# Optimization experiments

Measured on AMD Instinct MI355X. Metric: run time of the kernel, lower is better.

The kernel has to match this reference:

```python
import jax, jax.numpy as jnp
import numpy as np
from jax import lax

B, L, D_MODEL, N_LAYERS = 2, 1024, 768, 2
D_STATE, D_CONV, EXPAND = 16, 4, 2
ED = EXPAND * D_MODEL          # d_inner = 1536
DT_RANK = D_MODEL // 16        # 48
VOCAB = 32000                  # already multiple of 8


def setup_inputs() -> dict:
    key = jax.random.key(0)
    ks = jax.random.split(key, 12)
    s = 0.02
    # dt bias init: inverse-softplus of dt ~ LogUniform(dt_min, dt_max)
    dt = jnp.exp(jax.random.uniform(ks[0], (N_LAYERS, ED)) * (np.log(0.1) - np.log(0.001)) + np.log(0.001))
    dt = jnp.clip(dt, 1e-4)
    dt_b = dt + jnp.log(-jnp.expm1(-dt))
    A_log = jnp.tile(jnp.log(jnp.arange(1, D_STATE + 1, dtype=jnp.float32))[None, None, :], (N_LAYERS, ED, 1))
    return {
        "input_ids": jax.random.randint(ks[1], (B, L), 0, VOCAB),
        "embedding": jax.random.normal(ks[2], (VOCAB, D_MODEL)) * s,
        "ln_w": jnp.ones((N_LAYERS, D_MODEL)),
        "in_proj": jax.random.normal(ks[3], (N_LAYERS, 2 * ED, D_MODEL)) * s,
        "conv_w": jax.random.normal(ks[4], (N_LAYERS, ED, D_CONV)) * (1.0 / np.sqrt(D_CONV)),
        "conv_b": jnp.zeros((N_LAYERS, ED)),
        "x_proj": jax.random.normal(ks[5], (N_LAYERS, DT_RANK + 2 * D_STATE, ED)) * s,
        "dt_w": jax.random.normal(ks[6], (N_LAYERS, ED, DT_RANK)) * (DT_RANK ** -0.5),
        "dt_b": dt_b,
        "A_log": A_log,
        "skip_D": jnp.ones((N_LAYERS, ED)),
        "out_proj": jax.random.normal(ks[7], (N_LAYERS, D_MODEL, ED)) * s,
        "normf_w": jnp.ones((D_MODEL,)),
        "lm_head": jax.random.normal(ks[8], (VOCAB, D_MODEL)) * s,
    }


def _rmsnorm(x, w, eps=1e-5):
    return x * lax.rsqrt(jnp.mean(x * x, axis=-1, keepdims=True) + eps) * w


def _silu(x):
    return x * jax.nn.sigmoid(x)


def _mamba_layer(x, ln, w_in, cw, cb, w_x, wdt, bdt, a_log, d_skip, w_out):
    # x: (B, L, D)
    h = _rmsnorm(x, ln)
    xz = h @ w_in.T                               # (B, L, 2*ED)
    xi, z = xz[..., :ED], xz[..., ED:]
    # depthwise causal conv over time
    xc = jnp.pad(xi.transpose(0, 2, 1), ((0, 0), (0, 0), (D_CONV - 1, 0)))  # (B, ED, L+pad)
    xc = lax.conv_general_dilated(xc, cw[:, None, :], (1,), 'VALID',
                                  feature_group_count=ED,
                                  dimension_numbers=('NCH', 'OIH', 'NCH'))
    xi = _silu((xc + cb[None, :, None]).transpose(0, 2, 1))  # (B, L, ED)
    # input-dependent SSM params
    dbc = xi @ w_x.T                              # (B, L, dt_rank + 2N)
    delta_r = dbc[..., :DT_RANK]
    Bm = dbc[..., DT_RANK:DT_RANK + D_STATE]      # (B, L, N)
    Cm = dbc[..., DT_RANK + D_STATE:]             # (B, L, N)
    delta = jax.nn.softplus(delta_r @ wdt.T + bdt)  # (B, L, ED)
    A = -jnp.exp(a_log)                           # (ED, N)
    dA = jnp.exp(delta[..., None] * A)            # (B, L, ED, N)
    dBx = (delta * xi)[..., None] * Bm[:, :, None, :]  # (B, L, ED, N)

    def step(hc, t):
        dA_t, dBx_t, C_t = t
        hc = dA_t * hc + dBx_t                    # (B, ED, N)
        y = jnp.einsum('ben,bn->be', hc, C_t)
        return hc, y

    h0 = jnp.zeros((x.shape[0], ED, D_STATE), x.dtype)
    _, ys = lax.scan(step, h0, (dA.transpose(1, 0, 2, 3), dBx.transpose(1, 0, 2, 3), Cm.transpose(1, 0, 2)))
    y = ys.transpose(1, 0, 2) + d_skip * xi       # (B, L, ED)
    y = y * _silu(z)
    return x + y @ w_out.T                        # residual


def reference(input_ids, embedding, ln_w, in_proj, conv_w, conv_b, x_proj, dt_w, dt_b, A_log, skip_D, out_proj, normf_w, lm_head):
    x = embedding[input_ids]                      # (B, L, D)
    for i in range(N_LAYERS):
        x = _mamba_layer(x, ln_w[i], in_proj[i], conv_w[i], conv_b[i], x_proj[i],
                         dt_w[i], dt_b[i], A_log[i], skip_D[i], out_proj[i])
    x = _rmsnorm(x, normf_w)
    return x @ lm_head.T                          # (B, L, VOCAB)
```

## Files before the change

### kernel.cpp

```cpp
#include <hip/hip_runtime.h>
#include <hip/hip_bf16.h>

#define BB 2
#define LL 1024
#define DM 768
#define ED 1536
#define NTOK 2048
#define DSTATE 16
#define DTRANK 48
#define VOCAB 32000

#define CHUNK 64
#define NCHUNK (LL / CHUNK)

typedef unsigned short ushort_t;
typedef __attribute__((ext_vector_type(8))) short short8;
typedef __attribute__((ext_vector_type(4))) float f32x4;

__device__ __forceinline__ ushort_t f2bf(float f) {
    __hip_bfloat16 h = __float2bfloat16(f);
    return *(ushort_t*)&h;
}
__device__ __forceinline__ float silu(float x) { return x / (1.f + expf(-x)); }

__global__ void embed_kernel(const int* __restrict__ ids, const float* __restrict__ emb,
                             float* __restrict__ x) {
    int t = blockIdx.x;
    const float* src = emb + (size_t)ids[t] * DM;
    float* dst = x + (size_t)t * DM;
    for (int c = threadIdx.x; c < DM; c += blockDim.x) dst[c] = src[c];
}

__global__ void rmsnorm_kernel(const float* __restrict__ x, const float* __restrict__ w,
                               ushort_t* __restrict__ out, int D) {
    int t = blockIdx.x;
    const float* xr = x + (size_t)t * D;
    float ss = 0.f;
    for (int c = threadIdx.x; c < D; c += blockDim.x) { float v = xr[c]; ss += v * v; }
    #pragma unroll
    for (int o = 32; o > 0; o >>= 1) ss += __shfl_down(ss, o, 64);
    __shared__ float s[4];
    int wid = threadIdx.x >> 6;
    if ((threadIdx.x & 63) == 0) s[wid] = ss;
    __syncthreads();
    float rs = rsqrtf((s[0] + s[1] + s[2] + s[3]) / (float)D + 1e-5f);
    ushort_t* orow = out + (size_t)t * D;
    for (int c = threadIdx.x; c < D; c += blockDim.x)
        orow[c] = f2bf(xr[c] * rs * w[c]);
}

__global__ void w2bf_kernel(const float* __restrict__ w, ushort_t* __restrict__ o) {
    size_t i = ((size_t)blockIdx.x * blockDim.x + threadIdx.x) * 4;
    float4 f = *(const float4*)&w[i];
    ushort4 u;
    u.x = f2bf(f.x); u.y = f2bf(f.y); u.z = f2bf(f.z); u.w = f2bf(f.w);
    *(ushort4*)&o[i] = u;
}

template<bool RESID>
__global__ __launch_bounds__(256) void gemm_bt2(const ushort_t* __restrict__ A,
                                                const ushort_t* __restrict__ Wb,
                                                const float* X, float* out,
                                                int N, int K) {
    __shared__ __align__(16) ushort_t As[128 * 32];
    __shared__ __align__(16) ushort_t Bs[128 * 32];
    const int q = gridDim.x >> 3;
    const int f = (blockIdx.x & 7) * q + (blockIdx.x >> 3);
    const int m0 = (f & 15) * 128;
    const int n0 = (f >> 4) * 128;
    const int tid = threadIdx.x;
    const int w = tid >> 6, lane = tid & 63;
    const int wm = (w >> 1) * 64, wn = (w & 1) * 64;
    const int lrow = lane & 15, koff = (lane >> 4) * 8;
    const int srow = tid >> 2, scol = (tid & 3) * 8;
    const ushort_t* Ab = A  + (size_t)(m0 + srow) * K + scol;
    const ushort_t* Bb = Wb + (size_t)(n0 + srow) * K + scol;

    f32x4 acc[4][4] = {};

    for (int k0 = 0; k0 < K; k0 += 32) {
        uint4 a0 = *(const uint4*)(Ab + k0);
        uint4 a1 = *(const uint4*)(Ab + (size_t)64 * K + k0);
        uint4 b0 = *(const uint4*)(Bb + k0);
        uint4 b1 = *(const uint4*)(Bb + (size_t)64 * K + k0);
        __syncthreads();
        *(uint4*)&As[tid * 8]        = a0;
        *(uint4*)&As[2048 + tid * 8] = a1;
        *(uint4*)&Bs[tid * 8]        = b0;
        *(uint4*)&Bs[2048 + tid * 8] = b1;
        __syncthreads();
        short8 af[4], bfr[4];
        #pragma unroll
        for (int t = 0; t < 4; ++t) af[t]  = *(const short8*)&As[(wm + t * 16 + lrow) * 32 + koff];
        #pragma unroll
        for (int t = 0; t < 4; ++t) bfr[t] = *(const short8*)&Bs[(wn + t * 16 + lrow) * 32 + koff];
        #pragma unroll
        for (int tm = 0; tm < 4; ++tm)
            #pragma unroll
            for (int tn = 0; tn < 4; ++tn)
                acc[tm][tn] = __builtin_amdgcn_mfma_f32_16x16x32_bf16(af[tm], bfr[tn], acc[tm][tn], 0, 0, 0);
    }

    const int kq4 = (lane >> 4) * 4;
    #pragma unroll
    for (int tm = 0; tm < 4; ++tm) {
        #pragma unroll
        for (int tn = 0; tn < 4; ++tn) {
            const int c  = n0 + wn + tn * 16 + lrow;
            const int rb = m0 + wm + tm * 16 + kq4;
            #pragma unroll
            for (int i = 0; i < 4; ++i) {
                size_t off = (size_t)(rb + i) * N + c;
                float v = acc[tm][tn][i];
                if (RESID) v += X[off];
                out[off] = v;
            }
        }
    }
}

__global__ void conv_silu_kernel(const float* __restrict__ xz, const float* __restrict__ cw,
                                 const float* __restrict__ cb, float* __restrict__ xi) {
    int idx = blockIdx.x * blockDim.x + threadIdx.x;
    int c = idx % ED;
    int t = idx / ED;
    int l = t % LL;
    float acc = cb[c];
    #pragma unroll
    for (int k = 0; k < 4; ++k) {
        int ls = l + k - 3;
        if (ls >= 0) acc += xz[(size_t)(t + k - 3) * (2 * ED) + c] * cw[c * 4 + k];
    }
    xi[idx] = silu(acc);
}

__global__ void xproj_kernel(const float* __restrict__ xi, const float* __restrict__ wx,
                             float* __restrict__ dbc) {
    int t = blockIdx.x;
    __shared__ float sx[ED];
    const float* xr = xi + (size_t)t * ED;
    for (int c = threadIdx.x; c < ED; c += blockDim.x) sx[c] = xr[c];
    __syncthreads();
    int w = threadIdx.x >> 6, lane = threadIdx.x & 63;
    for (int j = w; j < DTRANK + 2 * DSTATE; j += 4) {
        const float* wr = wx + (size_t)j * ED;
        float s = 0.f;
        for (int k = lane; k < ED; k += 64) s += sx[k] * wr[k];
        #pragma unroll
        for (int o = 32; o > 0; o >>= 1) s += __shfl_down(s, o, 64);
        if (lane == 0) dbc[(size_t)t * 80 + j] = s;
    }
}

__global__ void dtproj_kernel(const float* __restrict__ dbc, const float* __restrict__ wdt,
                              const float* __restrict__ bdt, float* __restrict__ delta) {
    int t = blockIdx.x;
    __shared__ float sdr[DTRANK];
    if (threadIdx.x < DTRANK) sdr[threadIdx.x] = dbc[(size_t)t * 80 + threadIdx.x];
    __syncthreads();
    for (int e = threadIdx.x; e < ED; e += blockDim.x) {
        const float* wr = wdt + (size_t)e * DTRANK;
        float acc = bdt[e];
        #pragma unroll
        for (int r = 0; r < DTRANK; ++r) acc += sdr[r] * wr[r];
        delta[(size_t)t * ED + e] = (acc > 20.f) ? acc : log1pf(expf(acc));
    }
}


__global__ void scan_chunk_kernel(const float* __restrict__ delta, const float* __restrict__ xi,
                                  const float* __restrict__ dbc, const float* __restrict__ a_log,
                                  const float* __restrict__ skd, float* __restrict__ y,
                                  float* __restrict__ hfin, float* __restrict__ cA) {
    int b = blockIdx.z, c = blockIdx.y;
    int w = threadIdx.x >> 6, lane = threadIdx.x & 63;
    int n = lane & 15;
    int e = blockIdx.x * 16 + w * 4 + (lane >> 4);
    float Ae = -expf(a_log[e * DSTATE + n]);
    float skip = skd[e];
    float h = 0.f, sumdl = 0.f;
    size_t tb = (size_t)b * LL + (size_t)c * CHUNK;
    for (int l = 0; l < CHUNK; ++l) {
        size_t row = tb + l;
        float dl = delta[row * ED + e];
        float xv = xi[row * ED + e];
        float Bv = dbc[row * 80 + DTRANK + n];
        float Cv = dbc[row * 80 + DTRANK + DSTATE + n];
        float dA = __expf(dl * Ae);
        h = dA * h + dl * xv * Bv;
        sumdl += dl;
        float p = h * Cv;
        p += __shfl_xor(p, 1, 16);
        p += __shfl_xor(p, 2, 16);
        p += __shfl_xor(p, 4, 16);
        p += __shfl_xor(p, 8, 16);
        if (n == 0) y[row * ED + e] = p + skip * xv;
    }
    size_t sidx = (((size_t)b * NCHUNK + c) * ED + e) * DSTATE + n;
    hfin[sidx] = h;
    cA[sidx] = __expf(Ae * sumdl);
}

__global__ void chunk_carry_kernel(const float* __restrict__ hfin, const float* __restrict__ cA,
                                   float* __restrict__ hin) {
    int gid = blockIdx.x * blockDim.x + threadIdx.x;
    int b = gid / (ED * DSTATE);
    int rem = gid - b * (ED * DSTATE);
    float h = 0.f;
    for (int c = 0; c < NCHUNK; ++c) {
        size_t idx = ((size_t)(b * NCHUNK + c)) * (ED * DSTATE) + rem;
        hin[idx] = h;
        h = cA[idx] * h + hfin[idx];
    }
}

__global__ void scan_fixup_kernel(const float* __restrict__ delta, const float* __restrict__ dbc,
                                  const float* __restrict__ a_log, const float* __restrict__ hin,
                                  float* __restrict__ y) {
    int b = blockIdx.z, c = blockIdx.y + 1;
    int w = threadIdx.x >> 6, lane = threadIdx.x & 63;
    int n = lane & 15;
    int e = blockIdx.x * 16 + w * 4 + (lane >> 4);
    float Ae = -expf(a_log[e * DSTATE + n]);
    float h0 = hin[(((size_t)b * NCHUNK + c) * ED + e) * DSTATE + n];
    float sumdl = 0.f;
    size_t tb = (size_t)b * LL + (size_t)c * CHUNK;
    for (int l = 0; l < CHUNK; ++l) {
        size_t row = tb + l;
        float dl = delta[row * ED + e];
        sumdl += dl;
        float Cv = dbc[row * 80 + DTRANK + DSTATE + n];
        float p = __expf(Ae * sumdl) * h0 * Cv;
        p += __shfl_xor(p, 1, 16);
        p += __shfl_xor(p, 2, 16);
        p += __shfl_xor(p, 4, 16);
        p += __shfl_xor(p, 8, 16);
        if (n == 0) y[row * ED + e] += p;
    }
}

__global__ void gate_kernel(const float* __restrict__ y, const float* __restrict__ xz,
                            ushort_t* __restrict__ yzb) {
    int idx = blockIdx.x * blockDim.x + threadIdx.x;
    int c = idx % ED;
    int t = idx / ED;
    float z = xz[(size_t)t * (2 * ED) + ED + c];
    yzb[idx] = f2bf(y[idx] * silu(z));
}

extern "C" void kernel_launch(void* const* d_in, const int* in_sizes, int n_in,
                              void* d_out, int out_size, void* d_ws, size_t ws_size,
                              hipStream_t stream) {
    const int*   ids      = (const int*)d_in[0];
    const float* emb      = (const float*)d_in[1];
    const float* ln_w     = (const float*)d_in[2];
    const float* in_proj  = (const float*)d_in[3];
    const float* conv_w   = (const float*)d_in[4];
    const float* conv_b   = (const float*)d_in[5];
    const float* x_proj   = (const float*)d_in[6];
    const float* dt_w     = (const float*)d_in[7];
    const float* dt_b     = (const float*)d_in[8];
    const float* A_log    = (const float*)d_in[9];
    const float* skip_D   = (const float*)d_in[10];
    const float* out_proj = (const float*)d_in[11];
    const float* normf_w  = (const float*)d_in[12];
    const float* lm_head  = (const float*)d_in[13];

    char* ws = (char*)d_ws;
    float*    x     = (float*)(ws);
    ushort_t* h_bf  = (ushort_t*)(ws + 6291456);
    float*    xz    = (float*)(ws + 9437184);
    float*    xi    = (float*)(ws + 34603008);
    float*    dbc   = (float*)(ws + 47185920);
    float*    delta = (float*)(ws + 47841280);
    float*    y     = (float*)(ws + 60424192);
    ushort_t* yzb   = (ushort_t*)(ws + 73007104);
    float*    hfin  = (float*)(ws + 79298560);
    float*    cAbuf = (float*)(ws + 82444288);
    float*    hin   = (float*)h_bf;
    ushort_t* wip_bf = (ushort_t*)yzb;
    ushort_t* wo_bf  = (ushort_t*)xi;
    ushort_t* lmh_bf = (ushort_t*)xz;
    const size_t WS_NEED = 85590016;
    if (ws_size < WS_NEED) return;

    embed_kernel<<<NTOK, 256, 0, stream>>>(ids, emb, x);

    for (int i = 0; i < 2; ++i) {
        const float* lw   = ln_w + (size_t)i * DM;
        const float* wip  = in_proj + (size_t)i * 2 * ED * DM;
        const float* cw   = conv_w + (size_t)i * ED * 4;
        const float* cb   = conv_b + (size_t)i * ED;
        const float* wx   = x_proj + (size_t)i * 80 * ED;
        const float* wdt  = dt_w + (size_t)i * ED * DTRANK;
        const float* bdt  = dt_b + (size_t)i * ED;
        const float* alog = A_log + (size_t)i * ED * DSTATE;
        const float* skd  = skip_D + (size_t)i * ED;
        const float* wo   = out_proj + (size_t)i * DM * ED;

        rmsnorm_kernel<<<NTOK, 256, 0, stream>>>(x, lw, h_bf, DM);
        w2bf_kernel<<<2 * ED * DM / 1024, 256, 0, stream>>>(wip, wip_bf);
        gemm_bt2<false><<<16 * (2 * ED / 128), 256, 0, stream>>>(
            h_bf, wip_bf, nullptr, xz, 2 * ED, DM);
        conv_silu_kernel<<<NTOK * ED / 256, 256, 0, stream>>>(xz, cw, cb, xi);
        xproj_kernel<<<NTOK, 256, 0, stream>>>(xi, wx, dbc);
        dtproj_kernel<<<NTOK, 256, 0, stream>>>(dbc, wdt, bdt, delta);
        scan_chunk_kernel<<<dim3(ED / 16, NCHUNK, BB), 256, 0, stream>>>(
            delta, xi, dbc, alog, skd, y, hfin, cAbuf);
        chunk_carry_kernel<<<BB * ED * DSTATE / 256, 256, 0, stream>>>(hfin, cAbuf, hin);
        scan_fixup_kernel<<<dim3(ED / 16, NCHUNK - 1, BB), 256, 0, stream>>>(
            delta, dbc, alog, hin, y);
        w2bf_kernel<<<DM * ED / 1024, 256, 0, stream>>>(wo, wo_bf);
        gate_kernel<<<NTOK * ED / 256, 256, 0, stream>>>(y, xz, yzb);
        gemm_bt2<true><<<16 * (DM / 128), 256, 0, stream>>>(
            yzb, wo_bf, x, x, DM, ED);
    }

    rmsnorm_kernel<<<NTOK, 256, 0, stream>>>(x, normf_w, h_bf, DM);
    w2bf_kernel<<<VOCAB * DM / 1024, 256, 0, stream>>>(lm_head, lmh_bf);
    gemm_bt2<false><<<16 * (VOCAB / 128), 256, 0, stream>>>(
        h_bf, lmh_bf, nullptr, (float*)d_out, VOCAB, DM);
}
```

Baseline: 1.609 ms.

## Move x_proj to split-K bf16 MFMA GEMM and batch dt_proj over tokens

Replaces the per-token scalar x_proj dot-product kernel with a bf16 MFMA GEMM. The weights are padded to 128 rows and K is split eight ways, with partial results combined by atomicAdd into a zeroed dbc buffer. conv_silu now also writes a bf16 copy of xi to feed this GEMM. dt_proj now handles four tokens per block against a transposed weight for coalesced loads. The trade-off is bf16 rounding and nondeterministic atomic summation in the B/C/dt inputs, plus a few extra small kernels for weight conversion and zeroing.

```diff
diff --git a/kernel.cpp b/kernel.cpp
--- a/kernel.cpp
+++ b/kernel.cpp
@@ -12,6 +12,8 @@
 
 #define CHUNK 64
 #define NCHUNK (LL / CHUNK)
+
+#define XP_KS 8
 
 typedef unsigned short ushort_t;
 typedef __attribute__((ext_vector_type(8))) short short8;
@@ -55,6 +57,29 @@
     ushort4 u;
     u.x = f2bf(f.x); u.y = f2bf(f.y); u.z = f2bf(f.z); u.w = f2bf(f.w);
     *(ushort4*)&o[i] = u;
+}
+
+__global__ void wxpad_kernel(const float* __restrict__ wx, ushort_t* __restrict__ o) {
+    int i = (blockIdx.x * blockDim.x + threadIdx.x) * 4;
+    int row = i / ED;
+    ushort4 u;
+    if (row < 80) {
+        float4 f = *(const float4*)&wx[(size_t)row * ED + (i % ED)];
+        u.x = f2bf(f.x); u.y = f2bf(f.y); u.z = f2bf(f.z); u.w = f2bf(f.w);
+    } else {
+        u.x = u.y = u.z = u.w = 0;
+    }
+    *(ushort4*)&o[i] = u;
+}
+
+__global__ void wdtT_kernel(const float* __restrict__ wdt, float* __restrict__ wdtT) {
+    int id = blockIdx.x * blockDim.x + threadIdx.x;
+    int r = id / ED, e = id % ED;
+    wdtT[id] = wdt[(size_t)e * DTRANK + r];
+}
+
+__global__ void zero_dbc_kernel(float* __restrict__ dbc) {
+    dbc[blockIdx.x * blockDim.x + threadIdx.x] = 0.f;
 }
 
 template<bool RESID>
@@ -119,8 +144,69 @@
     }
 }
 
+__global__ __launch_bounds__(256) void gemm_xp(const ushort_t* __restrict__ A,
+                                               const ushort_t* __restrict__ Wb,
+                                               float* __restrict__ out) {
+    __shared__ __align__(16) ushort_t As[128 * 32];
+    __shared__ __align__(16) ushort_t Bs[128 * 32];
+    const int q = gridDim.x >> 3;
+    const int f = (blockIdx.x & 7) * q + (blockIdx.x >> 3);
+    const int m0 = (f & 15) * 128;
+    const int ks = f >> 4;
+    const int kbeg = ks * (ED / XP_KS);
+    const int kend = kbeg + ED / XP_KS;
+    const int tid = threadIdx.x;
+    const int w = tid >> 6, lane = tid & 63;
+    const int wm = (w >> 1) * 64, wn = (w & 1) * 64;
+    const int lrow = lane & 15, koff = (lane >> 4) * 8;
+    const int srow = tid >> 2, scol = (tid & 3) * 8;
+    const ushort_t* Ab = A  + (size_t)(m0 + srow) * ED + scol;
+    const ushort_t* Bb = Wb + (size_t)srow * ED + scol;
+
+    f32x4 acc[4][4] = {};
+
+    for (int k0 = kbeg; k0 < kend; k0 += 32) {
+        uint4 a0 = *(const uint4*)(Ab + k0);
+        uint4 a1 = *(const uint4*)(Ab + (size_t)64 * ED + k0);
+        uint4 b0 = *(const uint4*)(Bb + k0);
+        uint4 b1 = *(const uint4*)(Bb + (size_t)64 * ED + k0);
+        __syncthreads();
+        *(uint4*)&As[tid * 8]        = a0;
+        *(uint4*)&As[2048 + tid * 8] = a1;
+        *(uint4*)&Bs[tid * 8]        = b0;
+        *(uint4*)&Bs[2048 + tid * 8] = b1;
+        __syncthreads();
+        short8 af[4], bfr[4];
+        #pragma unroll
+        for (int t = 0; t < 4; ++t) af[t]  = *(const short8*)&As[(wm + t * 16 + lrow) * 32 + koff];
+        #pragma unroll
+        for (int t = 0; t < 4; ++t) bfr[t] = *(const short8*)&Bs[(wn + t * 16 + lrow) * 32 + koff];
+        #pragma unroll
+        for (int tm = 0; tm < 4; ++tm)
+            #pragma unroll
+            for (int tn = 0; tn < 4; ++tn)
+                acc[tm][tn] = __builtin_amdgcn_mfma_f32_16x16x32_bf16(af[tm], bfr[tn], acc[tm][tn], 0, 0, 0);
+    }
+
+    const int kq4 = (lane >> 4) * 4;
+    #pragma unroll
+    for (int tm = 0; tm < 4; ++tm) {
+        #pragma unroll
+        for (int tn = 0; tn < 4; ++tn) {
+            const int c  = wn + tn * 16 + lrow;
+            if (c < 80) {
+                const int rb = m0 + wm + tm * 16 + kq4;
+                #pragma unroll
+                for (int i = 0; i < 4; ++i)
+                    atomicAdd(&out[(size_t)(rb + i) * 80 + c], acc[tm][tn][i]);
+            }
+        }
+    }
+}
+
 __global__ void conv_silu_kernel(const float* __restrict__ xz, const float* __restrict__ cw,
-                                 const float* __restrict__ cb, float* __restrict__ xi) {
+                                 const float* __restrict__ cb, float* __restrict__ xi,
+                                 ushort_t* __restrict__ xib) {
     int idx = blockIdx.x * blockDim.x + threadIdx.x;
     int c = idx % ED;
     int t = idx / ED;
@@ -131,39 +217,35 @@
         int ls = l + k - 3;
         if (ls >= 0) acc += xz[(size_t)(t + k - 3) * (2 * ED) + c] * cw[c * 4 + k];
     }
-    xi[idx] = silu(acc);
-}
-
-__global__ void xproj_kernel(const float* __restrict__ xi, const float* __restrict__ wx,
-                             float* __restrict__ dbc) {
-    int t = blockIdx.x;
-    __shared__ float sx[ED];
-    const float* xr = xi + (size_t)t * ED;
-    for (int c = threadIdx.x; c < ED; c += blockDim.x) sx[c] = xr[c];
-    __syncthreads();
-    int w = threadIdx.x >> 6, lane = threadIdx.x & 63;
-    for (int j = w; j < DTRANK + 2 * DSTATE; j += 4) {
-        const float* wr = wx + (size_t)j * ED;
-        float s = 0.f;
-        for (int k = lane; k < ED; k += 64) s += sx[k] * wr[k];
-        #pragma unroll
-        for (int o = 32; o > 0; o >>= 1) s += __shfl_down(s, o, 64);
-        if (lane == 0) dbc[(size_t)t * 80 + j] = s;
-    }
-}
-
-__global__ void dtproj_kernel(const float* __restrict__ dbc, const float* __restrict__ wdt,
+    float v = silu(acc);
+    xi[idx] = v;
+    xib[idx] = f2bf(v);
+}
+
+#define DTT 4
+__global__ void dtproj_kernel(const float* __restrict__ dbc, const float* __restrict__ wdtT,
                               const float* __restrict__ bdt, float* __restrict__ delta) {
-    int t = blockIdx.x;
-    __shared__ float sdr[DTRANK];
-    if (threadIdx.x < DTRANK) sdr[threadIdx.x] = dbc[(size_t)t * 80 + threadIdx.x];
+    int t0 = blockIdx.x * DTT;
+    __shared__ float sdr[DTT][DTRANK];
+    if (threadIdx.x < DTT * DTRANK)
+        sdr[threadIdx.x / DTRANK][threadIdx.x % DTRANK] =
+            dbc[(size_t)(t0 + threadIdx.x / DTRANK) * 80 + (threadIdx.x % DTRANK)];
     __syncthreads();
     for (int e = threadIdx.x; e < ED; e += blockDim.x) {
-        const float* wr = wdt + (size_t)e * DTRANK;
-        float acc = bdt[e];
-        #pragma unroll
-        for (int r = 0; r < DTRANK; ++r) acc += sdr[r] * wr[r];
-        delta[(size_t)t * ED + e] = (acc > 20.f) ? acc : log1pf(expf(acc));
+        float b = bdt[e];
+        float a0 = b, a1 = b, a2 = b, a3 = b;
+        #pragma unroll
+        for (int r = 0; r < DTRANK; ++r) {
+            float wv = wdtT[r * ED + e];
+            a0 += sdr[0][r] * wv;
+            a1 += sdr[1][r] * wv;
+            a2 += sdr[2][r] * wv;
+            a3 += sdr[3][r] * wv;
+        }
+        delta[(size_t)(t0 + 0) * ED + e] = (a0 > 20.f) ? a0 : log1pf(expf(a0));
+        delta[(size_t)(t0 + 1) * ED + e] = (a1 > 20.f) ? a1 : log1pf(expf(a1));
+        delta[(size_t)(t0 + 2) * ED + e] = (a2 > 20.f) ? a2 : log1pf(expf(a2));
+        delta[(size_t)(t0 + 3) * ED + e] = (a3 > 20.f) ? a3 : log1pf(expf(a3));
     }
 }
 
@@ -277,10 +359,13 @@
     ushort_t* yzb   = (ushort_t*)(ws + 73007104);
     float*    hfin  = (float*)(ws + 79298560);
     float*    cAbuf = (float*)(ws + 82444288);
-    float*    hin   = (float*)h_bf;
+    float*    hin    = (float*)h_bf;
     ushort_t* wip_bf = (ushort_t*)yzb;
     ushort_t* wo_bf  = (ushort_t*)xi;
     ushort_t* lmh_bf = (ushort_t*)xz;
+    ushort_t* xib    = (ushort_t*)y;
+    ushort_t* wxb    = (ushort_t*)hfin;
+    float*    wdtT   = (float*)cAbuf;
     const size_t WS_NEED = 85590016;
     if (ws_size < WS_NEED) return;
 
@@ -302,9 +387,12 @@
         w2bf_kernel<<<2 * ED * DM / 1024, 256, 0, stream>>>(wip, wip_bf);
         gemm_bt2<false><<<16 * (2 * ED / 128), 256, 0, stream>>>(
             h_bf, wip_bf, nullptr, xz, 2 * ED, DM);
-        conv_silu_kernel<<<NTOK * ED / 256, 256, 0, stream>>>(xz, cw, cb, xi);
-        xproj_kernel<<<NTOK, 256, 0, stream>>>(xi, wx, dbc);
-        dtproj_kernel<<<NTOK, 256, 0, stream>>>(dbc, wdt, bdt, delta);
+        conv_silu_kernel<<<NTOK * ED / 256, 256, 0, stream>>>(xz, cw, cb, xi, xib);
+        wxpad_kernel<<<128 * ED / 1024, 256, 0, stream>>>(wx, wxb);
+        zero_dbc_kernel<<<NTOK * 80 / 256, 256, 0, stream>>>(dbc);
+        gemm_xp<<<16 * XP_KS, 256, 0, stream>>>(xib, wxb, dbc);
+        wdtT_kernel<<<DTRANK * ED / 256, 256, 0, stream>>>(wdt, wdtT);
+        dtproj_kernel<<<NTOK / DTT, 256, 0, stream>>>(dbc, wdtT, bdt, delta);
         scan_chunk_kernel<<<dim3(ED / 16, NCHUNK, BB), 256, 0, stream>>>(
             delta, xi, dbc, alog, skd, y, hfin, cAbuf);
         chunk_carry_kernel<<<BB * ED * DSTATE / 256, 256, 0, stream>>>(hfin, cAbuf, hin);
```

Result: faster. 1.345 ms (-16.4%).
